# Optimization experiments

Hardware: AMD Instinct MI355X
Metric: run time of the kernel (lower is better)

The kernel has to match this reference:

```python
import jax, jax.numpy as jnp
import numpy as np

_EPS = 1e-6
B, N, W, R, NW = 64, 1024, 64, 4, 1


def _cosine_weights(memory, keys, strengths):
    # memory: [B,N,W], keys: [B,H,W], strengths: [B,H] -> [B,H,N]
    dot = jnp.einsum('bhw,bnw->bhn', keys, memory)
    mem_norm = jnp.sqrt(jnp.sum(memory * memory, axis=-1) + _EPS)  # [B,N]
    key_norm = jnp.sqrt(jnp.sum(keys * keys, axis=-1) + _EPS)      # [B,H]
    sim = dot / (key_norm[:, :, None] * mem_norm[:, None, :] + _EPS)
    sharp = sim * jax.nn.softplus(strengths)[:, :, None]
    return jax.nn.softmax(sharp, axis=-1)


def _allocation(usage):
    # usage: [B,N] -> allocation weights [B,N] (DNC sort-based free-list)
    usage = _EPS + (1.0 - _EPS) * usage
    nonusage = 1.0 - usage
    sorted_nonusage, indices = jax.lax.top_k(nonusage, N)
    sorted_usage = 1.0 - sorted_nonusage
    prod_excl = jnp.concatenate(
        [jnp.ones_like(sorted_usage[:, :1]), jnp.cumprod(sorted_usage[:, :-1], axis=-1)], axis=-1)
    sorted_alloc = sorted_nonusage * prod_excl
    inv_perm = jnp.argsort(indices, axis=-1)  # batch_invert_permutation
    return jnp.take_along_axis(sorted_alloc, inv_perm, axis=-1)  # batch_gather


def _forward(memory, prev_read_weights, prev_write_weights, prev_usage, prev_link,
             prev_precedence, read_keys, read_strengths, write_keys, write_strengths,
             write_vectors, erase_vectors, free_gate, alloc_gate, write_gate, read_mode):
    # ---- usage update (Freeness.call); prev write weights are stop-gradient'd ----
    ww = jax.lax.stop_gradient(prev_write_weights)
    agg_write = 1.0 - jnp.prod(1.0 - ww, axis=1)                       # [B,N]
    usage = prev_usage + (1.0 - prev_usage) * agg_write
    phi = jnp.prod(1.0 - free_gate[:, :, None] * prev_read_weights, axis=1)
    usage = usage * phi
    # ---- write weights: content + allocation ----
    write_content = _cosine_weights(memory, write_keys, write_strengths)  # [B,NW,N]
    wg = alloc_gate * write_gate                                          # [B,NW]
    allocs = []
    u = usage
    for i in range(NW):  # fixed small head loop
        a = _allocation(u)
        allocs.append(a)
        u = u + (1.0 - u) * wg[:, i:i + 1] * a
    alloc_w = jnp.stack(allocs, axis=1)                                   # [B,NW,N]
    ag = alloc_gate[:, :, None]
    write_weights = write_gate[:, :, None] * (ag * alloc_w + (1.0 - ag) * write_content)
    # ---- erase + write memory ----
    reset = jnp.prod(1.0 - write_weights[:, :, :, None] * erase_vectors[:, :, None, :], axis=1)
    memory_new = memory * reset + jnp.einsum('bwn,bwk->bnk', write_weights, write_vectors)
    # ---- temporal link matrix update ----
    wi = write_weights[:, :, :, None]   # [B,NW,N,1]
    wj = write_weights[:, :, None, :]   # [B,NW,1,N]
    new_link = (1.0 - wi - wj) * prev_link + wi * prev_precedence[:, :, None, :]
    link = new_link * (1.0 - jnp.eye(N, dtype=memory.dtype))[None, None]  # zero diagonal
    # (precedence update, part of new state; not needed for read_words output)
    precedence = (1.0 - jnp.sum(write_weights, axis=-1, keepdims=True)) * prev_precedence + write_weights
    del precedence
    # ---- read weights: content + directional (forward/backward along link) ----
    read_content = _cosine_weights(memory_new, read_keys, read_strengths)   # [B,R,N]
    fwd_w = jnp.einsum('brm,bwnm->brwn', prev_read_weights, link)           # adjoint_b=True
    bwd_w = jnp.einsum('brm,bwmn->brwn', prev_read_weights, link)
    mode = jax.nn.softmax(read_mode, axis=-1)                                # [B,R,2*NW+1]
    backward_mode = mode[:, :, :NW]
    forward_mode = mode[:, :, NW:2 * NW]
    content_mode = mode[:, :, 2 * NW]
    read_weights = (content_mode[:, :, None] * read_content
                    + jnp.einsum('brw,brwn->brn', forward_mode, fwd_w)
                    + jnp.einsum('brw,brwn->brn', backward_mode, bwd_w))
    read_words = jnp.einsum('brn,bnw->brw', read_weights, memory_new)        # [B,R,W]
    return read_words


def setup_inputs() -> dict:
    key = jax.random.key(0)
    ks = jax.random.split(key, 16)
    rn = lambda k, s: jax.random.normal(k, s, jnp.float32)
    ru = lambda k, s: jax.random.uniform(k, s, dtype=jnp.float32)
    return {
        'memory': rn(ks[0], (B, N, W)),
        'prev_read_weights': ru(ks[1], (B, R, N)),
        'prev_write_weights': ru(ks[2], (B, NW, N)),
        'prev_usage': ru(ks[3], (B, N)),
        'prev_link': ru(ks[4], (B, NW, N, N)),
        'prev_precedence': ru(ks[5], (B, NW, N)),
        'read_keys': rn(ks[6], (B, R, W)),
        'read_strengths': rn(ks[7], (B, R)),
        'write_keys': rn(ks[8], (B, NW, W)),
        'write_strengths': rn(ks[9], (B, NW)),
        'write_vectors': rn(ks[10], (B, NW, W)),
        'erase_vectors': ru(ks[11], (B, NW, W)),
        'free_gate': ru(ks[12], (B, R)),
        'alloc_gate': ru(ks[13], (B, NW)),
        'write_gate': ru(ks[14], (B, NW)),
        'read_mode': rn(ks[15], (B, R, 2 * NW + 1)),
    }


def reference(memory, prev_read_weights, prev_write_weights, prev_usage, prev_link,
              prev_precedence, read_keys, read_strengths, write_keys, write_strengths,
              write_vectors, erase_vectors, free_gate, alloc_gate, write_gate, read_mode):
    return _forward(memory, prev_read_weights, prev_write_weights, prev_usage, prev_link,
                    prev_precedence, read_keys, read_strengths, write_keys, write_strengths,
                    write_vectors, erase_vectors, free_gate, alloc_gate, write_gate, read_mode)
```

## Files before the change

### kernel.cpp

```cpp
#include <hip/hip_runtime.h>
#include <cmath>

#define NN 1024
#define BB 64
#define WD 64
#define RR 4

constexpr float EPSF = 1e-6f;

__device__ __forceinline__ float softplusf(float x) {
    return fmaxf(x, 0.f) + log1pf(expf(-fabsf(x)));
}

__device__ __forceinline__ float block_sum(float v, float* red, float* bc) {
#pragma unroll
    for (int o = 1; o < 64; o <<= 1) v += __shfl_xor(v, o, 64);
    const int wid = threadIdx.x >> 6, lane = threadIdx.x & 63;
    if (lane == 0) red[wid] = v;
    __syncthreads();
    if (wid == 0) {
        float x = (lane < 16) ? red[lane] : 0.f;
#pragma unroll
        for (int o = 1; o < 16; o <<= 1) x += __shfl_xor(x, o, 64);
        if (lane == 0) bc[0] = x;
    }
    __syncthreads();
    return bc[0];
}

__device__ __forceinline__ float block_max(float v, float* red, float* bc) {
#pragma unroll
    for (int o = 1; o < 64; o <<= 1) v = fmaxf(v, __shfl_xor(v, o, 64));
    const int wid = threadIdx.x >> 6, lane = threadIdx.x & 63;
    if (lane == 0) red[wid] = v;
    __syncthreads();
    if (wid == 0) {
        float x = (lane < 16) ? red[lane] : -INFINITY;
#pragma unroll
        for (int o = 1; o < 16; o <<= 1) x = fmaxf(x, __shfl_xor(x, o, 64));
        if (lane == 0) bc[0] = x;
    }
    __syncthreads();
    return bc[0];
}

__device__ __forceinline__ float4 block_sum4(float4 v, float4* red, float4* bc) {
#pragma unroll
    for (int o = 1; o < 64; o <<= 1) {
        v.x += __shfl_xor(v.x, o, 64); v.y += __shfl_xor(v.y, o, 64);
        v.z += __shfl_xor(v.z, o, 64); v.w += __shfl_xor(v.w, o, 64);
    }
    const int wid = threadIdx.x >> 6, lane = threadIdx.x & 63;
    if (lane == 0) red[wid] = v;
    __syncthreads();
    if (wid == 0) {
        float4 x;
        if (lane < 16) x = red[lane];
        else { x.x = 0.f; x.y = 0.f; x.z = 0.f; x.w = 0.f; }
#pragma unroll
        for (int o = 1; o < 16; o <<= 1) {
            x.x += __shfl_xor(x.x, o, 64); x.y += __shfl_xor(x.y, o, 64);
            x.z += __shfl_xor(x.z, o, 64); x.w += __shfl_xor(x.w, o, 64);
        }
        if (lane == 0) bc[0] = x;
    }
    __syncthreads();
    return bc[0];
}

__device__ __forceinline__ float4 block_max4(float4 v, float4* red, float4* bc) {
#pragma unroll
    for (int o = 1; o < 64; o <<= 1) {
        v.x = fmaxf(v.x, __shfl_xor(v.x, o, 64)); v.y = fmaxf(v.y, __shfl_xor(v.y, o, 64));
        v.z = fmaxf(v.z, __shfl_xor(v.z, o, 64)); v.w = fmaxf(v.w, __shfl_xor(v.w, o, 64));
    }
    const int wid = threadIdx.x >> 6, lane = threadIdx.x & 63;
    if (lane == 0) red[wid] = v;
    __syncthreads();
    if (wid == 0) {
        float4 x;
        if (lane < 16) x = red[lane];
        else { x.x = -INFINITY; x.y = -INFINITY; x.z = -INFINITY; x.w = -INFINITY; }
#pragma unroll
        for (int o = 1; o < 16; o <<= 1) {
            x.x = fmaxf(x.x, __shfl_xor(x.x, o, 64)); x.y = fmaxf(x.y, __shfl_xor(x.y, o, 64));
            x.z = fmaxf(x.z, __shfl_xor(x.z, o, 64)); x.w = fmaxf(x.w, __shfl_xor(x.w, o, 64));
        }
        if (lane == 0) bc[0] = x;
    }
    __syncthreads();
    return bc[0];
}

#define COMP4(v4, c) ((c) == 0 ? (v4).x : ((c) == 1 ? (v4).y : ((c) == 2 ? (v4).z : (v4).w)))

__global__ __launch_bounds__(1024) void prep_kernel(
    const float* __restrict__ memory, const float* __restrict__ prw,
    const float* __restrict__ pww, const float* __restrict__ pusage,
    const float* __restrict__ pprec,
    const float* __restrict__ rkeys_g, const float* __restrict__ rstr_g,
    const float* __restrict__ wkeys_g, const float* __restrict__ wstr_g,
    const float* __restrict__ wvec_g, const float* __restrict__ evec_g,
    const float* __restrict__ fg_g, const float* __restrict__ ag_g,
    const float* __restrict__ wg_g,
    float* __restrict__ wwG, float* __restrict__ uwG, float* __restrict__ rcG,
    float* __restrict__ SrpG, float* __restrict__ SuwwG)
{
    __shared__ float wkey[WD], wvecS[WD], evecS[WD], rkey[RR * WD];
    __shared__ float skey[NN];
    __shared__ int   sidx[NN];
    __shared__ float pArr[NN], wcArr[NN], allocArr[NN];
    __shared__ float red1[16], bc1[1];
    __shared__ float4 red4[16], bc4[1];

    const int b = blockIdx.x, tid = threadIdx.x, n = tid;

    if (tid < WD) {
        wkey[tid]  = wkeys_g[b * WD + tid];
        wvecS[tid] = wvec_g[b * WD + tid];
        evecS[tid] = evec_g[b * WD + tid];
    } else if (tid >= 128 && tid < 128 + RR * WD) {
        int k = tid - 128;
        rkey[k] = rkeys_g[b * RR * WD + k];
    }
    __syncthreads();

    float ur[RR];
#pragma unroll
    for (int r = 0; r < RR; ++r) ur[r] = prw[((size_t)b * RR + r) * NN + n];
    const float pw = pww[b * NN + n];
    const float pu = pusage[b * NN + n];
    float usage = pu + (1.f - pu) * pw;
    float phi = 1.f;
#pragma unroll
    for (int r = 0; r < RR; ++r) phi *= (1.f - fg_g[b * RR + r] * ur[r]);
    usage *= phi;

    const float* mrow = memory + ((size_t)b * NN + n) * WD;
    float dot = 0.f, nrm = 0.f, knrm = 0.f;
#pragma unroll 4
    for (int w4 = 0; w4 < WD / 4; ++w4) {
        const float4 m = *(const float4*)(mrow + w4 * 4);
        const float4 k = *(const float4*)(wkey + w4 * 4);
        dot  += m.x * k.x + m.y * k.y + m.z * k.z + m.w * k.w;
        nrm  += m.x * m.x + m.y * m.y + m.z * m.z + m.w * m.w;
        knrm += k.x * k.x + k.y * k.y + k.z * k.z + k.w * k.w;
    }
    const float sim = dot / (sqrtf(knrm + EPSF) * sqrtf(nrm + EPSF) + EPSF);
    const float sharp = sim * softplusf(wstr_g[b]);
    const float mxw = block_max(sharp, red1, bc1);
    const float exw = expf(sharp - mxw);
    const float smw = block_sum(exw, red1, bc1);
    wcArr[n] = exw / smw;

    const float ue = EPSF + (1.f - EPSF) * usage;
    skey[n] = 1.f - ue;
    sidx[n] = n;
    __syncthreads();
    for (int k = 2; k <= NN; k <<= 1) {
        for (int j = k >> 1; j > 0; j >>= 1) {
            const int ixj = tid ^ j;
            if (ixj > tid) {
                const float ka = skey[tid], kb = skey[ixj];
                const int ia = sidx[tid], ib = sidx[ixj];
                const bool precBA = (kb > ka) || (kb == ka && ib < ia);
                const bool precAB = (ka > kb) || (ka == kb && ia < ib);
                const bool dosw = ((tid & k) == 0) ? precBA : precAB;
                if (dosw) { skey[tid] = kb; skey[ixj] = ka; sidx[tid] = ib; sidx[ixj] = ia; }
            }
            __syncthreads();
        }
    }
    pArr[n] = (n == 0) ? 1.f : (1.f - skey[n - 1]);
    __syncthreads();
    for (int off = 1; off < NN; off <<= 1) {
        const float t = (n >= off) ? pArr[n - off] : 1.f;
        __syncthreads();
        pArr[n] *= t;
        __syncthreads();
    }
    allocArr[sidx[n]] = skey[n] * pArr[n];
    __syncthreads();

    const float agv = ag_g[b], wgv = wg_g[b];
    const float ww = wgv * (agv * allocArr[n] + (1.f - agv) * wcArr[n]);
    wwG[b * NN + n] = ww;
#pragma unroll
    for (int r = 0; r < RR; ++r)
        uwG[((size_t)b * RR + r) * NN + n] = ur[r] * ww;

    float rdot0 = 0, rdot1 = 0, rdot2 = 0, rdot3 = 0, nn2 = 0;
    float rk0 = 0, rk1 = 0, rk2 = 0, rk3 = 0;
#pragma unroll 4
    for (int w4 = 0; w4 < WD / 4; ++w4) {
        const float4 m = *(const float4*)(mrow + w4 * 4);
        const float4 e = *(const float4*)(evecS + w4 * 4);
        const float4 v = *(const float4*)(wvecS + w4 * 4);
        float4 mn_;
        mn_.x = m.x * (1.f - ww * e.x) + ww * v.x;
        mn_.y = m.y * (1.f - ww * e.y) + ww * v.y;
        mn_.z = m.z * (1.f - ww * e.z) + ww * v.z;
        mn_.w = m.w * (1.f - ww * e.w) + ww * v.w;
        nn2 += mn_.x * mn_.x + mn_.y * mn_.y + mn_.z * mn_.z + mn_.w * mn_.w;
        const float4 k0 = *(const float4*)(rkey + 0 * WD + w4 * 4);
        const float4 k1 = *(const float4*)(rkey + 1 * WD + w4 * 4);
        const float4 k2 = *(const float4*)(rkey + 2 * WD + w4 * 4);
        const float4 k3 = *(const float4*)(rkey + 3 * WD + w4 * 4);
        rdot0 += k0.x * mn_.x + k0.y * mn_.y + k0.z * mn_.z + k0.w * mn_.w;
        rdot1 += k1.x * mn_.x + k1.y * mn_.y + k1.z * mn_.z + k1.w * mn_.w;
        rdot2 += k2.x * mn_.x + k2.y * mn_.y + k2.z * mn_.z + k2.w * mn_.w;
        rdot3 += k3.x * mn_.x + k3.y * mn_.y + k3.z * mn_.z + k3.w * mn_.w;
        rk0 += k0.x * k0.x + k0.y * k0.y + k0.z * k0.z + k0.w * k0.w;
        rk1 += k1.x * k1.x + k1.y * k1.y + k1.z * k1.z + k1.w * k1.w;
        rk2 += k2.x * k2.x + k2.y * k2.y + k2.z * k2.z + k2.w * k2.w;
        rk3 += k3.x * k3.x + k3.y * k3.y + k3.z * k3.z + k3.w * k3.w;
    }
    const float mnn = sqrtf(nn2 + EPSF);
    float4 sharp4;
    sharp4.x = rdot0 / (sqrtf(rk0 + EPSF) * mnn + EPSF) * softplusf(rstr_g[b * RR + 0]);
    sharp4.y = rdot1 / (sqrtf(rk1 + EPSF) * mnn + EPSF) * softplusf(rstr_g[b * RR + 1]);
    sharp4.z = rdot2 / (sqrtf(rk2 + EPSF) * mnn + EPSF) * softplusf(rstr_g[b * RR + 2]);
    sharp4.w = rdot3 / (sqrtf(rk3 + EPSF) * mnn + EPSF) * softplusf(rstr_g[b * RR + 3]);
    const float4 mx4 = block_max4(sharp4, red4, bc4);
    float4 e4;
    e4.x = expf(sharp4.x - mx4.x); e4.y = expf(sharp4.y - mx4.y);
    e4.z = expf(sharp4.z - mx4.z); e4.w = expf(sharp4.w - mx4.w);
    const float4 s4 = block_sum4(e4, red4, bc4);
    rcG[((size_t)b * RR + 0) * NN + n] = e4.x / s4.x;
    rcG[((size_t)b * RR + 1) * NN + n] = e4.y / s4.y;
    rcG[((size_t)b * RR + 2) * NN + n] = e4.z / s4.z;
    rcG[((size_t)b * RR + 3) * NN + n] = e4.w / s4.w;

    const float prec_n = pprec[b * NN + n];
    float4 sp4, sw4;
    sp4.x = ur[0] * prec_n; sp4.y = ur[1] * prec_n; sp4.z = ur[2] * prec_n; sp4.w = ur[3] * prec_n;
    const float4 SrpV = block_sum4(sp4, red4, bc4);
    sw4.x = ur[0] * ww; sw4.y = ur[1] * ww; sw4.z = ur[2] * ww; sw4.w = ur[3] * ww;
    const float4 SuwwV = block_sum4(sw4, red4, bc4);
    if (tid == 0) {
        SrpG[b * RR + 0] = SrpV.x; SrpG[b * RR + 1] = SrpV.y;
        SrpG[b * RR + 2] = SrpV.z; SrpG[b * RR + 3] = SrpV.w;
        SuwwG[b * RR + 0] = SuwwV.x; SuwwG[b * RR + 1] = SuwwV.y;
        SuwwG[b * RR + 2] = SuwwV.z; SuwwG[b * RR + 3] = SuwwV.w;
    }
}

__global__ __launch_bounds__(256, 2) void link_kernel(
    const float* __restrict__ L, const float* __restrict__ uG,
    const float* __restrict__ uwG,
    float* __restrict__ rowU, float* __restrict__ rowV,
    float* __restrict__ colU, float* __restrict__ colV)
{
    __shared__ float tile[64 * 132];

    const int b = blockIdx.y;
    const int n0 = blockIdx.x * 64;
    const int t = threadIdx.x;
    const int lane = t & 63;
    const int wid = t >> 6;
    const int widu = __builtin_amdgcn_readfirstlane(wid);

    const float* uR  = uG  + ((size_t)b * RR + widu) * NN;
    const float* uwR = uwG + ((size_t)b * RR + widu) * NN;

    const int q = lane >> 4;
    float4 ucol[4], uwcol[4];
#pragma unroll
    for (int j4 = 0; j4 < 4; ++j4) {
        ucol[j4]  = *(const float4*)(uR  + n0 + q * 16 + j4 * 4);
        uwcol[j4] = *(const float4*)(uwR + n0 + q * 16 + j4 * 4);
    }

    const float* Lb = L + (size_t)b * NN * NN + (size_t)n0 * NN;
    const int srow = t >> 5;
    const int sc4  = (t & 31) << 2;

    float4 pre[8];
#pragma unroll
    for (int k = 0; k < 8; ++k)
        pre[k] = *(const float4*)&Lb[(size_t)(srow + (k << 3)) * NN + sc4];
#pragma unroll
    for (int k = 0; k < 8; ++k)
        *(float4*)&tile[(srow + (k << 3)) * 132 + sc4] = pre[k];

    float fuA = 0.f, fvA = 0.f;
    const int c16 = (lane & 15) << 2;

    for (int tt = 0; tt < 8; ++tt) {
        __syncthreads();
        if (tt < 7) {
#pragma unroll
            for (int k = 0; k < 8; ++k)
                pre[k] = *(const float4*)&Lb[(size_t)(srow + (k << 3)) * NN + ((tt + 1) << 7) + sc4];
        }

        const int m0 = tt << 7;

#pragma unroll
        for (int g = 0; g < 32; ++g) {
            const float4 v  = *(const float4*)&tile[lane * 132 + (g << 2)];
            const float4 u  = *(const float4*)(uR  + m0 + (g << 2));
            const float4 uw = *(const float4*)(uwR + m0 + (g << 2));
            fuA += v.x * u.x + v.y * u.y + v.z * u.z + v.w * u.w;
            fvA += v.x * uw.x + v.y * uw.y + v.z * uw.z + v.w * uw.w;
        }

#pragma unroll
        for (int h = 0; h < 2; ++h) {
            float4 cu4 = {0.f, 0.f, 0.f, 0.f}, cv4 = {0.f, 0.f, 0.f, 0.f};
#pragma unroll
            for (int j = 0; j < 16; ++j) {
                const int row = q * 16 + j;
                const float4 v = *(const float4*)&tile[row * 132 + (h << 6) + c16];
                const float uv  = COMP4(ucol[j >> 2],  j & 3);
                const float uwv = COMP4(uwcol[j >> 2], j & 3);
                cu4.x += uv * v.x;  cu4.y += uv * v.y;  cu4.z += uv * v.z;  cu4.w += uv * v.w;
                cv4.x += uwv * v.x; cv4.y += uwv * v.y; cv4.z += uwv * v.z; cv4.w += uwv * v.w;
            }
#pragma unroll
            for (int off = 16; off < 64; off <<= 1) {
                cu4.x += __shfl_xor(cu4.x, off, 64); cu4.y += __shfl_xor(cu4.y, off, 64);
                cu4.z += __shfl_xor(cu4.z, off, 64); cu4.w += __shfl_xor(cu4.w, off, 64);
                cv4.x += __shfl_xor(cv4.x, off, 64); cv4.y += __shfl_xor(cv4.y, off, 64);
                cv4.z += __shfl_xor(cv4.z, off, 64); cv4.w += __shfl_xor(cv4.w, off, 64);
            }
            const int src = lane >> 2, cc = lane & 3;
            const float gx = __shfl(cu4.x, src, 64), gy = __shfl(cu4.y, src, 64);
            const float gz = __shfl(cu4.z, src, 64), gw = __shfl(cu4.w, src, 64);
            const float cuS = (cc == 0) ? gx : ((cc == 1) ? gy : ((cc == 2) ? gz : gw));
            const float hx = __shfl(cv4.x, src, 64), hy = __shfl(cv4.y, src, 64);
            const float hz = __shfl(cv4.z, src, 64), hw = __shfl(cv4.w, src, 64);
            const float cvS = (cc == 0) ? hx : ((cc == 1) ? hy : ((cc == 2) ? hz : hw));
            unsafeAtomicAdd(&colU[((size_t)b * RR + wid) * NN + m0 + (h << 6) + lane], cuS);
            unsafeAtomicAdd(&colV[((size_t)b * RR + wid) * NN + m0 + (h << 6) + lane], cvS);
        }

        __syncthreads();
        if (tt < 7) {
#pragma unroll
            for (int k = 0; k < 8; ++k)
                *(float4*)&tile[(srow + (k << 3)) * 132 + sc4] = pre[k];
        }
    }
    rowU[((size_t)b * RR + wid) * NN + n0 + lane] = fuA;
    rowV[((size_t)b * RR + wid) * NN + n0 + lane] = fvA;
}

__global__ __launch_bounds__(256) void combine_kernel(
    const float* __restrict__ memory, const float* __restrict__ prw,
    const float* __restrict__ pprec, const float* __restrict__ L,
    const float* __restrict__ evec_g, const float* __restrict__ wvec_g,
    const float* __restrict__ rmode_g,
    const float* __restrict__ wwG, const float* __restrict__ rcG,
    const float* __restrict__ rowU, const float* __restrict__ rowV,
    const float* __restrict__ colU, const float* __restrict__ colV,
    const float* __restrict__ SrpG, const float* __restrict__ SuwwG,
    float* __restrict__ out)
{
    __shared__ float rwL[RR][64];
    __shared__ float wwS[64];

    const int b = blockIdx.y;
    const int n0 = blockIdx.x * 64;
    const int t = threadIdx.x;
    const int r = t >> 6, i = t & 63;
    const int n = n0 + i;

    const float wwn = wwG[b * NN + n];
    if (r == 0) wwS[i] = wwn;
    const float prec_n = pprec[b * NN + n];
    const float diag = L[(size_t)b * NN * NN + (size_t)n * (NN + 1)];

    {
        const size_t idx = ((size_t)b * RR + r) * NN + n;
        const float un = prw[idx];
        const float rc = rcG[idx];
        const float ru = rowU[idx], rv = rowV[idx];
        const float cuv = colU[idx], cvv = colV[idx];
        const float Srp = SrpG[b * RR + r], Suww = SuwwG[b * RR + r];
        const float corr = un * (1.f - 2.f * wwn) * diag;
        const float fwd = (1.f - wwn) * ru - rv - corr + wwn * (Srp - un * prec_n);
        const float bwd = (1.f - wwn) * cuv - cvv - corr + prec_n * (Suww - un * wwn);
        const float m0 = rmode_g[((size_t)b * RR + r) * 3 + 0];
        const float m1 = rmode_g[((size_t)b * RR + r) * 3 + 1];
        const float m2 = rmode_g[((size_t)b * RR + r) * 3 + 2];
        const float mx = fmaxf(m0, fmaxf(m1, m2));
        const float e0 = expf(m0 - mx), e1 = expf(m1 - mx), e2 = expf(m2 - mx);
        const float inv = 1.f / (e0 + e1 + e2);
        rwL[r][i] = (e2 * inv) * rc + (e1 * inv) * fwd + (e0 * inv) * bwd;
    }
    __syncthreads();

    const int w = i;
    const float ev = evec_g[b * WD + w], wv = wvec_g[b * WD + w];
    float acc = 0.f;
    const float* mb = memory + ((size_t)b * NN + n0) * WD;
#pragma unroll 8
    for (int k = 0; k < 64; ++k) {
        const float m = mb[(size_t)k * WD + w];
        const float wwi = wwS[k];
        acc += rwL[r][k] * (m * (1.f - wwi * ev) + wwi * wv);
    }
    unsafeAtomicAdd(&out[((size_t)b * RR + r) * WD + w], acc);
}

extern "C" void kernel_launch(void* const* d_in, const int* in_sizes, int n_in,
                              void* d_out, int out_size, void* d_ws, size_t ws_size,
                              hipStream_t stream) {
    const float* memory = (const float*)d_in[0];
    const float* prw    = (const float*)d_in[1];
    const float* pww    = (const float*)d_in[2];
    const float* pusage = (const float*)d_in[3];
    const float* plink  = (const float*)d_in[4];
    const float* pprec  = (const float*)d_in[5];
    const float* rkeys  = (const float*)d_in[6];
    const float* rstr   = (const float*)d_in[7];
    const float* wkeys  = (const float*)d_in[8];
    const float* wstr   = (const float*)d_in[9];
    const float* wvec   = (const float*)d_in[10];
    const float* evec   = (const float*)d_in[11];
    const float* fg     = (const float*)d_in[12];
    const float* ag     = (const float*)d_in[13];
    const float* wg     = (const float*)d_in[14];
    const float* rmode  = (const float*)d_in[15];

    float* ws = (float*)d_ws;
    const size_t BN  = (size_t)BB * NN;
    const size_t BRN = (size_t)BB * RR * NN;
    float* wwG  = ws;
    float* rcG  = wwG + BN;
    float* uwG  = rcG + BRN;
    float* rowU = uwG + BRN;
    float* rowV = rowU + BRN;
    float* colU = rowV + BRN;
    float* colV = colU + BRN;
    float* Srp  = colV + BRN;
    float* Suww = Srp + (size_t)BB * RR;

    hipMemsetAsync(colU, 0, 2 * BRN * sizeof(float), stream);
    hipMemsetAsync(d_out, 0, (size_t)out_size * sizeof(float), stream);

    prep_kernel<<<BB, 1024, 0, stream>>>(memory, prw, pww, pusage, pprec,
                                         rkeys, rstr, wkeys, wstr, wvec, evec,
                                         fg, ag, wg, wwG, uwG, rcG, Srp, Suww);
    link_kernel<<<dim3(16, BB), 256, 0, stream>>>(plink, prw, uwG,
                                                  rowU, rowV, colU, colV);
    combine_kernel<<<dim3(16, BB), 256, 0, stream>>>(memory, prw, pprec, plink,
                                                     evec, wvec, rmode,
                                                     wwG, rcG, rowU, rowV, colU, colV,
                                                     Srp, Suww, (float*)d_out);
}
```

Measured before the change: 571.7 us.

## Replace column atomics with per-stripe partial buffers reduced in combine kernel

The link kernel now writes its column partial sums for each 64-row stripe into a separate slice of a partials buffer using plain float4 stores, instead of float atomic adds into one shared colU/colV array. The combine kernel sums the 16 partial slices. This removes the atomic traffic and the memset of the column buffers. The cost is a much larger workspace and extra reads in combine, and the old atomic path is kept as a fallback when the workspace is too small. Launch bounds also move from 2 to 3 waves per EU hint.

```diff
diff --git a/kernel.cpp b/kernel.cpp
--- a/kernel.cpp
+++ b/kernel.cpp
@@ -245,7 +245,8 @@
     }
 }
 
-__global__ __launch_bounds__(256, 2) void link_kernel(
+template <bool PART>
+__global__ __launch_bounds__(256, 3) void link_kernel(
     const float* __restrict__ L, const float* __restrict__ uG,
     const float* __restrict__ uwG,
     float* __restrict__ rowU, float* __restrict__ rowV,
@@ -324,15 +325,25 @@
                 cv4.x += __shfl_xor(cv4.x, off, 64); cv4.y += __shfl_xor(cv4.y, off, 64);
                 cv4.z += __shfl_xor(cv4.z, off, 64); cv4.w += __shfl_xor(cv4.w, off, 64);
             }
-            const int src = lane >> 2, cc = lane & 3;
-            const float gx = __shfl(cu4.x, src, 64), gy = __shfl(cu4.y, src, 64);
-            const float gz = __shfl(cu4.z, src, 64), gw = __shfl(cu4.w, src, 64);
-            const float cuS = (cc == 0) ? gx : ((cc == 1) ? gy : ((cc == 2) ? gz : gw));
-            const float hx = __shfl(cv4.x, src, 64), hy = __shfl(cv4.y, src, 64);
-            const float hz = __shfl(cv4.z, src, 64), hw = __shfl(cv4.w, src, 64);
-            const float cvS = (cc == 0) ? hx : ((cc == 1) ? hy : ((cc == 2) ? hz : hw));
-            unsafeAtomicAdd(&colU[((size_t)b * RR + wid) * NN + m0 + (h << 6) + lane], cuS);
-            unsafeAtomicAdd(&colV[((size_t)b * RR + wid) * NN + m0 + (h << 6) + lane], cvS);
+
+            if (PART) {
+                if (lane < 16) {
+                    const size_t cb = ((((size_t)blockIdx.x * BB + b) * RR + wid) * NN)
+                                      + m0 + (h << 6) + (lane << 2);
+                    *(float4*)&colU[cb] = cu4;
+                    *(float4*)&colV[cb] = cv4;
+                }
+            } else {
+                const int src = lane >> 2, cc = lane & 3;
+                const float gx = __shfl(cu4.x, src, 64), gy = __shfl(cu4.y, src, 64);
+                const float gz = __shfl(cu4.z, src, 64), gw = __shfl(cu4.w, src, 64);
+                const float cuS = (cc == 0) ? gx : ((cc == 1) ? gy : ((cc == 2) ? gz : gw));
+                const float hx = __shfl(cv4.x, src, 64), hy = __shfl(cv4.y, src, 64);
+                const float hz = __shfl(cv4.z, src, 64), hw = __shfl(cv4.w, src, 64);
+                const float cvS = (cc == 0) ? hx : ((cc == 1) ? hy : ((cc == 2) ? hz : hw));
+                unsafeAtomicAdd(&colU[((size_t)b * RR + wid) * NN + m0 + (h << 6) + lane], cuS);
+                unsafeAtomicAdd(&colV[((size_t)b * RR + wid) * NN + m0 + (h << 6) + lane], cvS);
+            }
         }
 
         __syncthreads();
@@ -355,6 +366,7 @@
     const float* __restrict__ rowU, const float* __restrict__ rowV,
     const float* __restrict__ colU, const float* __restrict__ colV,
     const float* __restrict__ SrpG, const float* __restrict__ SuwwG,
+    int nPart, size_t partStride,
     float* __restrict__ out)
 {
     __shared__ float rwL[RR][64];
@@ -376,7 +388,11 @@
         const float un = prw[idx];
         const float rc = rcG[idx];
         const float ru = rowU[idx], rv = rowV[idx];
-        const float cuv = colU[idx], cvv = colV[idx];
+        float cuv = 0.f, cvv = 0.f;
+        for (int s = 0; s < nPart; ++s) {
+            cuv += colU[(size_t)s * partStride + idx];
+            cvv += colV[(size_t)s * partStride + idx];
+        }
         const float Srp = SrpG[b * RR + r], Suww = SuwwG[b * RR + r];
         const float corr = un * (1.f - 2.f * wwn) * diag;
         const float fwd = (1.f - wwn) * ru - rv - corr + wwn * (Srp - un * prec_n);
@@ -427,26 +443,45 @@
     float* ws = (float*)d_ws;
     const size_t BN  = (size_t)BB * NN;
     const size_t BRN = (size_t)BB * RR * NN;
+    const int NSTRIPE = 16;
+
     float* wwG  = ws;
     float* rcG  = wwG + BN;
     float* uwG  = rcG + BRN;
     float* rowU = uwG + BRN;
     float* rowV = rowU + BRN;
-    float* colU = rowV + BRN;
-    float* colV = colU + BRN;
-    float* Srp  = colV + BRN;
+    float* Srp  = rowV + BRN;
     float* Suww = Srp + (size_t)BB * RR;
-
-    hipMemsetAsync(colU, 0, 2 * BRN * sizeof(float), stream);
-    hipMemsetAsync(d_out, 0, (size_t)out_size * sizeof(float), stream);
+    float* cols = Suww + (size_t)BB * RR;
+
+    const size_t needPart = (size_t)(cols - ws) + 2 * (size_t)NSTRIPE * BRN;
+    const bool usePart = ws_size >= needPart * sizeof(float);
 
     prep_kernel<<<BB, 1024, 0, stream>>>(memory, prw, pww, pusage, pprec,
                                          rkeys, rstr, wkeys, wstr, wvec, evec,
                                          fg, ag, wg, wwG, uwG, rcG, Srp, Suww);
-    link_kernel<<<dim3(16, BB), 256, 0, stream>>>(plink, prw, uwG,
-                                                  rowU, rowV, colU, colV);
-    combine_kernel<<<dim3(16, BB), 256, 0, stream>>>(memory, prw, pprec, plink,
-                                                     evec, wvec, rmode,
-                                                     wwG, rcG, rowU, rowV, colU, colV,
-                                                     Srp, Suww, (float*)d_out);
-}
+    hipMemsetAsync(d_out, 0, (size_t)out_size * sizeof(float), stream);
+
+    if (usePart) {
+        float* colPU = cols;
+        float* colPV = colPU + (size_t)NSTRIPE * BRN;
+        link_kernel<true><<<dim3(NSTRIPE, BB), 256, 0, stream>>>(plink, prw, uwG,
+                                                                 rowU, rowV, colPU, colPV);
+        combine_kernel<<<dim3(16, BB), 256, 0, stream>>>(memory, prw, pprec, plink,
+                                                         evec, wvec, rmode,
+                                                         wwG, rcG, rowU, rowV, colPU, colPV,
+                                                         Srp, Suww, NSTRIPE, BRN,
+                                                         (float*)d_out);
+    } else {
+        float* colU = cols;
+        float* colV = colU + BRN;
+        hipMemsetAsync(colU, 0, 2 * BRN * sizeof(float), stream);
+        link_kernel<false><<<dim3(NSTRIPE, BB), 256, 0, stream>>>(plink, prw, uwG,
+                                                                  rowU, rowV, colU, colV);
+        combine_kernel<<<dim3(16, BB), 256, 0, stream>>>(memory, prw, pprec, plink,
+                                                         evec, wvec, rmode,
+                                                         wwG, rcG, rowU, rowV, colU, colV,
+                                                         Srp, Suww, 1, 0,
+                                                         (float*)d_out);
+    }
+}
```

Measured after the change: 841.4 us. 47.2% more time.
